# Kernel tuning notes

Measured on AMD Instinct MI355X. Metric: run time of the kernel, lower is better.

Reference implementation:

```python
import jax, jax.numpy as jnp
import numpy as np


def setup_inputs() -> dict:
    key = jax.random.key(0)
    k1, k2, k3 = jax.random.split(key, 3)
    B, T, F = 8, 4096, 512
    feat = jax.random.normal(k1, (B, T, F), dtype=jnp.float32)
    # nn.Linear(n_feat, 1): weight [1, F] -> store as [F] vector, bias scalar [1]
    W = jax.random.normal(k2, (F,), dtype=jnp.float32) * (1.0 / np.sqrt(F))
    b = jax.random.normal(k3, (1,), dtype=jnp.float32) * 0.1
    return {"feat": feat, "W": W, "b": b}


def reference(feat, W, b):
    # feat: [B, T, F]
    B, T, F = feat.shape
    # Linear(F->1) + sigmoid -> per-frame score [B, T]
    score = jax.nn.sigmoid(jnp.einsum("btf,f->bt", feat, W) + b[0])
    # neighbor scores with edge replication (matches torch cat pattern)
    score_left = jnp.concatenate([score[:, :1], score[:, :-1]], axis=1)
    score_right = jnp.concatenate([score[:, 1:], score[:, -1:]], axis=1)
    peaks = (score >= score_left) & (score >= score_right)  # [B, T] bool
    hlens = jnp.sum(peaks, axis=1).astype(jnp.int32)  # [B]
    # Stream compaction: stable argsort puts peak indices first, in order.
    order = jnp.argsort(~peaks, axis=1, stable=True)  # [B, T] int
    gathered = jnp.take_along_axis(feat, order[:, :, None], axis=1)  # [B, T, F]
    valid = jnp.arange(T, dtype=jnp.int32)[None, :] < hlens[:, None]  # [B, T]
    # Zero out padded tail (torch pre-zeros feat_new). NOTE: padded to T (static
    # upper bound) instead of data-dependent max(hlens), for jit compatibility;
    # rows beyond max(hlens) are all-zero.
    feat_new = jnp.where(valid[:, :, None], gathered, jnp.zeros((), feat.dtype))
    return feat_new, hlens
```

## Files before the change

kernel.cpp:

```cpp
#include <hip/hip_runtime.h>
#include <hip/hip_bf16.h>


#define T_DIM 4096
#define F_DIM 512
#define B_DIM 8

__global__ void __launch_bounds__(256) score_kernel(
    const float* __restrict__ feat, const float* __restrict__ W,
    const float* __restrict__ bias, float* __restrict__ score, int nrows) {
  int gtid = blockIdx.x * blockDim.x + threadIdx.x;
  int row  = gtid >> 6;
  int lane = threadIdx.x & 63;
  if (row >= nrows) return;

  const float4* fr = (const float4*)(feat + (size_t)row * F_DIM);
  const float4* wv = (const float4*)W;
  int i0 = lane * 2;
  float4 a0 = fr[i0];
  float4 a1 = fr[i0 + 1];
  float4 w0 = wv[i0];
  float4 w1 = wv[i0 + 1];
  float sum = a0.x * w0.x + a0.y * w0.y + a0.z * w0.z + a0.w * w0.w
            + a1.x * w1.x + a1.y * w1.y + a1.z * w1.z + a1.w * w1.w;

  #pragma unroll
  for (int d = 32; d > 0; d >>= 1) sum += __shfl_xor(sum, d, 64);

  if (lane == 0) {
    float x = sum + bias[0];
    score[row] = 1.0f / (1.0f + expf(-x));
  }
}

__global__ void __launch_bounds__(1024) peaks_scan_kernel(
    const float* __restrict__ score, int* __restrict__ idx,
    int* __restrict__ hlens_i, float* __restrict__ hlens_f) {
  int b = blockIdx.x;
  __shared__ float s[T_DIM];
  __shared__ int wsum[16];

  const float* sb = score + b * T_DIM;
  int tid = threadIdx.x;

  ((float4*)s)[tid] = ((const float4*)sb)[tid];
  __syncthreads();

  int t0 = tid * 4;
  int flags[4];
  int cnt = 0;
  #pragma unroll
  for (int j = 0; j < 4; j++) {
    int t = t0 + j;
    float c = s[t];
    float l = (t == 0) ? c : s[t - 1];
    float r = (t == T_DIM - 1) ? c : s[t + 1];
    flags[j] = (c >= l && c >= r) ? 1 : 0;
    cnt += flags[j];
  }

  int lane = tid & 63;
  int wave = tid >> 6;
  int inc = cnt;
  #pragma unroll
  for (int d = 1; d < 64; d <<= 1) {
    int v = __shfl_up(inc, d, 64);
    if (lane >= d) inc += v;
  }
  if (lane == 63) wsum[wave] = inc;
  __syncthreads();

  if (tid == 0) {
    int acc = 0;
    #pragma unroll
    for (int w = 0; w < 16; w++) { int v = wsum[w]; wsum[w] = acc; acc += v; }
    hlens_i[b] = acc;
    hlens_f[b] = (float)acc;
  }
  __syncthreads();

  int base = wsum[wave] + inc - cnt;
  int* ib = idx + b * T_DIM;
  #pragma unroll
  for (int j = 0; j < 4; j++) {
    if (flags[j]) ib[base++] = t0 + j;
  }
}

__global__ void __launch_bounds__(256) gather_kernel(
    const float* __restrict__ feat, const int* __restrict__ idx,
    const int* __restrict__ hlens_i, float* __restrict__ out, int nrows) {
  int gtid = blockIdx.x * blockDim.x + threadIdx.x;
  int row  = gtid >> 6;
  int lane = threadIdx.x & 63;
  if (row >= nrows) return;

  int b = row >> 12;
  int d = row & (T_DIM - 1);
  float4* orow = (float4*)(out + (size_t)row * F_DIM);
  int i0 = lane * 2;

  if (d < hlens_i[b]) {
    int src = idx[row];
    const float4* fr = (const float4*)(feat + ((size_t)(b << 12) + src) * F_DIM);
    orow[i0]     = fr[i0];
    orow[i0 + 1] = fr[i0 + 1];
  } else {
    float4 z = make_float4(0.f, 0.f, 0.f, 0.f);
    orow[i0]     = z;
    orow[i0 + 1] = z;
  }
}

extern "C" void kernel_launch(void* const* d_in, const int* in_sizes, int n_in,
                              void* d_out, int out_size, void* d_ws, size_t ws_size,
                              hipStream_t stream) {
  const float* feat = (const float*)d_in[0];
  const float* W    = (const float*)d_in[1];
  const float* bias = (const float*)d_in[2];

  float* out       = (float*)d_out;
  float* hlens_f   = out + (size_t)B_DIM * T_DIM * F_DIM;

  float* score   = (float*)d_ws;
  int*   idx     = (int*)((char*)d_ws + 32768 * 4);
  int*   hlens_i = (int*)((char*)d_ws + 32768 * 8);

  const int nrows = B_DIM * T_DIM;

  score_kernel<<<nrows / 4, 256, 0, stream>>>(feat, W, bias, score, nrows);

  peaks_scan_kernel<<<B_DIM, 1024, 0, stream>>>(score, idx, hlens_i, hlens_f);

  gather_kernel<<<nrows / 4, 256, 0, stream>>>(feat, idx, hlens_i, out, nrows);
}
```

Measured before the change: 119.5 us.

## Fuse peak scan and gather into one kernel with redundant per-slice scans

Merges the peak-detection scan and the gather into one kernel launched with 32 blocks per batch. Each block recomputes the full per-batch prefix scan in shared memory, writes the compacted indices to LDS, and then copies or zeroes its 128-row slice of the output. This removes one kernel launch, the global idx/hlens round trip and the serial 8-block scan stage. In exchange the scan runs 32 times per batch, and the gather now uses 1024-thread blocks with 8 rows per wave.

Measured after the change: 115.4 us. -3.4%, faster.

```diff
diff --git a/kernel.cpp b/kernel.cpp
--- a/kernel.cpp
+++ b/kernel.cpp
@@ -33,17 +33,22 @@
   }
 }
 
-__global__ void __launch_bounds__(1024) peaks_scan_kernel(
-    const float* __restrict__ score, int* __restrict__ idx,
-    int* __restrict__ hlens_i, float* __restrict__ hlens_f) {
-  int b = blockIdx.x;
+__global__ void __launch_bounds__(1024) scan_gather_kernel(
+    const float* __restrict__ feat, const float* __restrict__ score,
+    float* __restrict__ out, float* __restrict__ hlens_f) {
+  int b     = blockIdx.x >> 5;
+  int slice = blockIdx.x & 31;
+
   __shared__ float s[T_DIM];
-  __shared__ int wsum[16];
+  __shared__ int   wsum[16];
+  __shared__ int   total_s;
+  int* sidx = (int*)s;
 
-  const float* sb = score + b * T_DIM;
-  int tid = threadIdx.x;
+  int tid  = threadIdx.x;
+  int lane = tid & 63;
+  int wave = tid >> 6;
 
-  ((float4*)s)[tid] = ((const float4*)sb)[tid];
+  ((float4*)s)[tid] = ((const float4*)(score + b * T_DIM))[tid];
   __syncthreads();
 
   int t0 = tid * 4;
@@ -59,8 +64,6 @@
     cnt += flags[j];
   }
 
-  int lane = tid & 63;
-  int wave = tid >> 6;
   int inc = cnt;
   #pragma unroll
   for (int d = 1; d < 64; d <<= 1) {
@@ -74,41 +77,37 @@
     int acc = 0;
     #pragma unroll
     for (int w = 0; w < 16; w++) { int v = wsum[w]; wsum[w] = acc; acc += v; }
-    hlens_i[b] = acc;
-    hlens_f[b] = (float)acc;
+    total_s = acc;
+    if (slice == 0) hlens_f[b] = (float)acc;
   }
   __syncthreads();
 
   int base = wsum[wave] + inc - cnt;
-  int* ib = idx + b * T_DIM;
   #pragma unroll
   for (int j = 0; j < 4; j++) {
-    if (flags[j]) ib[base++] = t0 + j;
+    if (flags[j]) sidx[base++] = t0 + j;
   }
-}
+  __syncthreads();
 
-__global__ void __launch_bounds__(256) gather_kernel(
-    const float* __restrict__ feat, const int* __restrict__ idx,
-    const int* __restrict__ hlens_i, float* __restrict__ out, int nrows) {
-  int gtid = blockIdx.x * blockDim.x + threadIdx.x;
-  int row  = gtid >> 6;
-  int lane = threadIdx.x & 63;
-  if (row >= nrows) return;
+  int total = total_s;
 
-  int b = row >> 12;
-  int d = row & (T_DIM - 1);
-  float4* orow = (float4*)(out + (size_t)row * F_DIM);
-  int i0 = lane * 2;
-
-  if (d < hlens_i[b]) {
-    int src = idx[row];
-    const float4* fr = (const float4*)(feat + ((size_t)(b << 12) + src) * F_DIM);
-    orow[i0]     = fr[i0];
-    orow[i0 + 1] = fr[i0 + 1];
-  } else {
-    float4 z = make_float4(0.f, 0.f, 0.f, 0.f);
-    orow[i0]     = z;
-    orow[i0 + 1] = z;
+  const float* fb = feat + (size_t)b * T_DIM * F_DIM;
+  float*       ob = out  + (size_t)b * T_DIM * F_DIM;
+  #pragma unroll
+  for (int r = 0; r < 8; r++) {
+    int d = slice * 128 + wave * 8 + r;
+    float4* orow = (float4*)(ob + (size_t)d * F_DIM);
+    if (d < total) {
+      const float4* fr = (const float4*)(fb + (size_t)sidx[d] * F_DIM);
+      float4 v0 = fr[lane];
+      float4 v1 = fr[lane + 64];
+      orow[lane]      = v0;
+      orow[lane + 64] = v1;
+    } else {
+      float4 z = make_float4(0.f, 0.f, 0.f, 0.f);
+      orow[lane]      = z;
+      orow[lane + 64] = z;
+    }
   }
 }
 
@@ -119,18 +118,14 @@
   const float* W    = (const float*)d_in[1];
   const float* bias = (const float*)d_in[2];
 
-  float* out       = (float*)d_out;
-  float* hlens_f   = out + (size_t)B_DIM * T_DIM * F_DIM;
+  float* out     = (float*)d_out;
+  float* hlens_f = out + (size_t)B_DIM * T_DIM * F_DIM;
 
-  float* score   = (float*)d_ws;
-  int*   idx     = (int*)((char*)d_ws + 32768 * 4);
-  int*   hlens_i = (int*)((char*)d_ws + 32768 * 8);
+  float* score = (float*)d_ws;
 
   const int nrows = B_DIM * T_DIM;
 
   score_kernel<<<nrows / 4, 256, 0, stream>>>(feat, W, bias, score, nrows);
 
-  peaks_scan_kernel<<<B_DIM, 1024, 0, stream>>>(score, idx, hlens_i, hlens_f);
-
-  gather_kernel<<<nrows / 4, 256, 0, stream>>>(feat, idx, hlens_i, out, nrows);
+  scan_gather_kernel<<<B_DIM * 32, 1024, 0, stream>>>(feat, score, out, hlens_f);
 }
```
